# Optimization experiments

Hardware: AMD Instinct MI355X
Metric: run time of the kernel (lower is better)

The kernel has to match this reference:

```python
import jax, jax.numpy as jnp
import numpy as np

N = 100000   # nodes
D = 64       # in_features
E = 1200000  # edges (avg degree ~12)
C = 1.0      # curvature
MIN_NORM = 1e-15
PROJ_EPS = 4e-3  # float32 eps used by HGCN-style PoincareBall.proj


def setup_inputs() -> dict:
    key = jax.random.key(0)
    k1, k2, k3 = jax.random.split(key, 3)
    x = jax.random.normal(k1, (N, D), dtype=jnp.float32) * 0.1
    edge_index = jax.random.randint(k2, (2, E), 0, N, dtype=jnp.int32)
    # GCNConv learned params (lin weight + bias)
    W = jax.random.normal(k3, (D, D), dtype=jnp.float32) / np.sqrt(D)
    b = jnp.zeros((D,), dtype=jnp.float32)
    return {"x": x, "W": W, "b": b, "edge_index": edge_index}


def expmap0(u, c):
    sqrt_c = jnp.sqrt(c)
    u_norm = jnp.maximum(jnp.linalg.norm(u, axis=-1, keepdims=True), MIN_NORM)
    return jnp.tanh(sqrt_c * u_norm) * u / (sqrt_c * u_norm)


def proj(x, c):
    norm = jnp.maximum(jnp.linalg.norm(x, axis=-1, keepdims=True), MIN_NORM)
    maxnorm = (1.0 - PROJ_EPS) / jnp.sqrt(c)
    return jnp.where(norm > maxnorm, x / norm * maxnorm, x)


def gcn_conv(x, W, b, edge_index, n_nodes):
    # PyG GCNConv: h = x @ W; add self-loops; symmetric normalization; scatter-add; + bias
    h = x @ W  # [N, D]
    src, dst = edge_index[0], edge_index[1]
    loops = jnp.arange(n_nodes, dtype=edge_index.dtype)
    s = jnp.concatenate([src, loops])  # [E+N]
    d = jnp.concatenate([dst, loops])
    deg = jax.ops.segment_sum(jnp.ones(s.shape, dtype=h.dtype), d, num_segments=n_nodes)
    deg_inv_sqrt = jnp.where(deg > 0, deg ** -0.5, 0.0)
    norm = deg_inv_sqrt[s] * deg_inv_sqrt[d]  # [E+N]
    msgs = h[s] * norm[:, None]               # gather + scale: [E+N, D]
    out = jax.ops.segment_sum(msgs, d, num_segments=n_nodes)  # scatter-add
    return out + b


def reference(x, W, b, edge_index):
    # Note: original computes logmap0(x) but discards it (conv uses raw x) -- dead code.
    support_t = gcn_conv(x, W, b, edge_index, N)
    return proj(expmap0(support_t, C), C)
```

## Files before the change

kernel.cpp:

```cpp
#include <hip/hip_runtime.h>
#include <hip/hip_bf16.h>

#define DFEAT 64
#define NBSH  8
#define NPB   256
#define EPB   8192

__global__ __launch_bounds__(256) void histA_kernel(const int* __restrict__ ei,
                                                    int* __restrict__ blkhist, int E) {
    __shared__ int h[512];
    int t = threadIdx.x;
    h[t] = 0; h[t + 256] = 0;
    __syncthreads();
    int base = blockIdx.x * EPB;
    #pragma unroll
    for (int i = 0; i < EPB / 256; ++i) {
        int e = base + i * 256 + t;
        if (e < E) atomicAdd(&h[ei[E + e] >> NBSH], 1);
    }
    __syncthreads();
    blkhist[blockIdx.x * 512 + t]       = h[t];
    blkhist[blockIdx.x * 512 + t + 256] = h[t + 256];
}

__global__ __launch_bounds__(512) void scanB_kernel(int* __restrict__ blkhist,
                                                    int* __restrict__ bucketbase, int nblk) {
    __shared__ int lds[512];
    int t = threadIdx.x;
    int run = 0;
    for (int blk = 0; blk < nblk; ++blk) {
        int idx = blk * 512 + t;
        int v = blkhist[idx];
        blkhist[idx] = run;
        run += v;
    }
    lds[t] = run;
    __syncthreads();
    int s = run;
    for (int off = 1; off < 512; off <<= 1) {
        int y = (t >= off) ? lds[t - off] : 0;
        __syncthreads();
        lds[t] += y;
        __syncthreads();
    }
    bucketbase[t] = lds[t] - s;
}

__global__ __launch_bounds__(256) void partC_kernel(const int* __restrict__ ei,
                                                    const int* __restrict__ blkhist,
                                                    const int* __restrict__ bucketbase,
                                                    unsigned* __restrict__ ebuf, int E) {
    __shared__ int cur[512];
    int t = threadIdx.x;
    cur[t]       = bucketbase[t]       + blkhist[blockIdx.x * 512 + t];
    cur[t + 256] = bucketbase[t + 256] + blkhist[blockIdx.x * 512 + t + 256];
    __syncthreads();
    int base = blockIdx.x * EPB;
    #pragma unroll
    for (int i = 0; i < EPB / 256; ++i) {
        int e = base + i * 256 + t;
        if (e < E) {
            int s = ei[e];
            int d = ei[E + e];
            int pos = atomicAdd(&cur[d >> NBSH], 1);
            ebuf[pos] = (unsigned)s | ((unsigned)(d & (NPB - 1)) << 17);
        }
    }
}

__global__ __launch_bounds__(256) void csrD_kernel(const unsigned* __restrict__ ebuf,
                                                   const int* __restrict__ bucketbase,
                                                   int* __restrict__ srcs,
                                                   int* __restrict__ begs,
                                                   int* __restrict__ lens,
                                                   float* __restrict__ dinv, int n) {
    __shared__ int cnt[256];
    __shared__ int tmp[256];
    int t = threadIdx.x;
    int b = blockIdx.x;
    int ebeg = bucketbase[b], eend = bucketbase[b + 1];
    int regionbase = ebeg + b * (4 * NPB);
    cnt[t] = 0;
    __syncthreads();
    for (int e = ebeg + t; e < eend; e += 256)
        atomicAdd(&cnt[ebuf[e] >> 17], 1);
    __syncthreads();
    int nid = (b << NBSH) + t;
    int deg = cnt[t];
    int slots = (nid < n) ? ((deg + 4) & ~3) : 0;
    tmp[t] = slots;
    __syncthreads();
    int s = slots;
    for (int o = 1; o < 256; o <<= 1) {
        int y = (t >= o) ? tmp[t - o] : 0;
        __syncthreads();
        tmp[t] += y;
        __syncthreads();
    }
    int excl = tmp[t] - s;
    if (nid < n) {
        int beg_abs = regionbase + excl;
        begs[nid] = beg_abs;
        lens[nid] = slots;
        dinv[nid] = rsqrtf((float)(deg + 1));
        srcs[beg_abs] = nid;
        for (int k = deg + 1; k < slots; ++k) srcs[beg_abs + k] = n;
    }
    cnt[t] = excl + 1;
    __syncthreads();
    for (int e = ebeg + t; e < eend; e += 256) {
        unsigned v = ebuf[e];
        int pos = atomicAdd(&cnt[v >> 17], 1);
        srcs[regionbase + pos] = (int)(v & 0x1ffffu);
    }
}

__global__ __launch_bounds__(256) void xsprep_kernel(const float* __restrict__ x,
                                                     const float* __restrict__ dinv,
                                                     unsigned* __restrict__ xs, int n) {
    int i = blockIdx.x * blockDim.x + threadIdx.x;
    int total = (n + 1) * 32;
    if (i >= total) return;
    int row = i >> 5, col = i & 31;
    unsigned v = 0;
    if (row < n) {
        float di = dinv[row];
        float f0 = x[row * DFEAT + 2 * col] * di;
        float f1 = x[row * DFEAT + 2 * col + 1] * di;
        unsigned u0 = __float_as_uint(f0); u0 = (u0 + 0x7fffu + ((u0 >> 16) & 1u)) >> 16;
        unsigned u1 = __float_as_uint(f1); u1 = (u1 + 0x7fffu + ((u1 >> 16) & 1u)) >> 16;
        v = (u0 & 0xffffu) | (u1 << 16);
    }
    xs[i] = v;
}

__global__ __launch_bounds__(256) void agg_kernel(const int* __restrict__ begs,
                                                  const int* __restrict__ lens,
                                                  const int* __restrict__ srcs,
                                                  const float* __restrict__ dinv,
                                                  const uint2* __restrict__ xs2,
                                                  const float* __restrict__ W,
                                                  const float* __restrict__ b,
                                                  float* __restrict__ out,
                                                  int n, int nquads) {
    __shared__ float Wl[DFEAT * DFEAT];
    __shared__ float xl[4][DFEAT];
    int t = threadIdx.x;
    #pragma unroll
    for (int i = 0; i < 16; ++i) Wl[i * 256 + t] = W[i * 256 + t];
    __syncthreads();

    int r = t >> 6, lane = t & 63;
    int g = lane >> 4;
    int q = lane & 15;
    float bias = b[lane];

    for (int quad = blockIdx.x; quad < nquads; quad += gridDim.x) {
        int node = quad * 4 + r;
        if (node >= n) continue;

        float f0 = 0, f1 = 0, f2 = 0, f3 = 0;
        int beg = begs[node];
        int end = beg + lens[node];
        for (int base = beg; base < end; base += 64) {
            int m = end - base; if (m > 64) m = 64;
            int idx = 0;
            if (lane < m) idx = srcs[base + lane];
            int quads_ = m >> 2;
            for (int j = 0; j < quads_; ++j) {
                int sv = __shfl(idx, 4 * j + g, 64);
                uint2 d = xs2[(unsigned)sv * 16 + q];
                f0 += __uint_as_float(d.x << 16);
                f1 += __uint_as_float(d.x & 0xffff0000u);
                f2 += __uint_as_float(d.y << 16);
                f3 += __uint_as_float(d.y & 0xffff0000u);
            }
        }
        #pragma unroll
        for (int off = 16; off < 64; off <<= 1) {
            f0 += __shfl_xor(f0, off, 64);
            f1 += __shfl_xor(f1, off, 64);
            f2 += __shfl_xor(f2, off, 64);
            f3 += __shfl_xor(f3, off, 64);
        }
        if (g == 0) {
            float di = dinv[node];
            xl[r][4 * q + 0] = f0 * di;
            xl[r][4 * q + 1] = f1 * di;
            xl[r][4 * q + 2] = f2 * di;
            xl[r][4 * q + 3] = f3 * di;
        }

        float o0 = bias, o1 = 0.0f;
        #pragma unroll
        for (int k = 0; k < DFEAT; k += 2) {
            o0 = fmaf(xl[r][k],     Wl[k * DFEAT + lane],       o0);
            o1 = fmaf(xl[r][k + 1], Wl[(k + 1) * DFEAT + lane], o1);
        }
        float o = o0 + o1;

        float ss = o * o;
        #pragma unroll
        for (int off = 32; off > 0; off >>= 1) ss += __shfl_xor(ss, off, 64);
        float norm = fmaxf(sqrtf(ss), 1e-15f);
        float tn = tanhf(norm);
        float scale = fminf(tn, 1.0f - 4e-3f) / norm;
        out[(long long)node * DFEAT + lane] = o * scale;
    }
}


extern "C" void kernel_launch(void* const* d_in, const int* in_sizes, int n_in,
                              void* d_out, int out_size, void* d_ws, size_t ws_size,
                              hipStream_t stream) {
    const float* x = (const float*)d_in[0];
    const float* W = (const float*)d_in[1];
    const float* b = (const float*)d_in[2];
    const int* ei  = (const int*)d_in[3];

    int n = in_sizes[0] / DFEAT;
    int E = in_sizes[3] / 2;
    int NB = (n + NPB - 1) / NPB;
    int nblk = (E + EPB - 1) / EPB;
    int nquads = (n + 3) / 4;

    int* blkhist    = (int*)d_ws;
    int* bucketbase = blkhist + nblk * 512;
    int* srcs       = bucketbase + 512;
    int* begs       = srcs + E + NB * 4 * NPB;
    int* lens       = begs + n;
    float* dinv     = (float*)(lens + n);
    unsigned* ebuf  = (unsigned*)(dinv + n);
    unsigned* xs    = ebuf;

    float* out = (float*)d_out;

    int aggblocks = 2048;
    if (aggblocks > nquads) aggblocks = nquads;

    histA_kernel <<<nblk, 256, 0, stream>>>(ei, blkhist, E);
    scanB_kernel <<<1, 512, 0, stream>>>(blkhist, bucketbase, nblk);
    partC_kernel <<<nblk, 256, 0, stream>>>(ei, blkhist, bucketbase, ebuf, E);
    csrD_kernel  <<<NB, 256, 0, stream>>>(ebuf, bucketbase, srcs, begs, lens, dinv, n);
    xsprep_kernel<<<((n + 1) * 32 + 255) / 256, 256, 0, stream>>>(x, dinv, xs, n);
    agg_kernel   <<<aggblocks, 256, 0, stream>>>(begs, lens, srcs, dinv,
                                                 (const uint2*)xs, W, b, out, n, nquads);
}
```

Before: 225.6 us.

## Parallelize bucket scan, fuse bf16 prep into CSR build, widen gathers to 16 bytes

The single-block serial scan over all per-block histograms is replaced by a transposed histogram layout, a 512-block per-bucket scan, and a small scan over bucket totals. The xsprep kernel is folded into csrD, which now scales and packs its own rows using dinv held in shared memory. This removes a launch and a reread of dinv. The aggregation kernel loads 8 bf16 features per lane (uint4) for 8 edges per step instead of 4, with a tail path for groups of four. It also gives xs its own aligned workspace region so it no longer aliases ebuf.

After: 228.9 us. About the same (+1.4%).

```diff
diff --git a/kernel.cpp b/kernel.cpp
--- a/kernel.cpp
+++ b/kernel.cpp
@@ -7,7 +7,8 @@
 #define EPB   8192
 
 __global__ __launch_bounds__(256) void histA_kernel(const int* __restrict__ ei,
-                                                    int* __restrict__ blkhist, int E) {
+                                                    int* __restrict__ blkhistT,
+                                                    int E, int nblk) {
     __shared__ int h[512];
     int t = threadIdx.x;
     h[t] = 0; h[t + 256] = 0;
@@ -19,24 +20,37 @@
         if (e < E) atomicAdd(&h[ei[E + e] >> NBSH], 1);
     }
     __syncthreads();
-    blkhist[blockIdx.x * 512 + t]       = h[t];
-    blkhist[blockIdx.x * 512 + t + 256] = h[t + 256];
-}
-
-__global__ __launch_bounds__(512) void scanB_kernel(int* __restrict__ blkhist,
-                                                    int* __restrict__ bucketbase, int nblk) {
+    blkhistT[t * nblk + blockIdx.x]         = h[t];
+    blkhistT[(t + 256) * nblk + blockIdx.x] = h[t + 256];
+}
+
+__global__ __launch_bounds__(256) void scanB1_kernel(int* __restrict__ blkhistT,
+                                                     int* __restrict__ buckettotal, int nblk) {
+    __shared__ int lds[256];
+    int t = threadIdx.x;
+    int b = blockIdx.x;
+    int v = (t < nblk) ? blkhistT[b * nblk + t] : 0;
+    lds[t] = v;
+    __syncthreads();
+    #pragma unroll
+    for (int off = 1; off < 256; off <<= 1) {
+        int y = (t >= off) ? lds[t - off] : 0;
+        __syncthreads();
+        lds[t] += y;
+        __syncthreads();
+    }
+    if (t < nblk) blkhistT[b * nblk + t] = lds[t] - v;
+    if (t == 255) buckettotal[b] = lds[255];
+}
+
+__global__ __launch_bounds__(512) void scanB2_kernel(const int* __restrict__ buckettotal,
+                                                     int* __restrict__ bucketbase) {
     __shared__ int lds[512];
     int t = threadIdx.x;
-    int run = 0;
-    for (int blk = 0; blk < nblk; ++blk) {
-        int idx = blk * 512 + t;
-        int v = blkhist[idx];
-        blkhist[idx] = run;
-        run += v;
-    }
-    lds[t] = run;
-    __syncthreads();
-    int s = run;
+    int s = buckettotal[t];
+    lds[t] = s;
+    __syncthreads();
+    #pragma unroll
     for (int off = 1; off < 512; off <<= 1) {
         int y = (t >= off) ? lds[t - off] : 0;
         __syncthreads();
@@ -44,16 +58,17 @@
         __syncthreads();
     }
     bucketbase[t] = lds[t] - s;
+    if (t == 511) bucketbase[512] = lds[511];
 }
 
 __global__ __launch_bounds__(256) void partC_kernel(const int* __restrict__ ei,
-                                                    const int* __restrict__ blkhist,
+                                                    const int* __restrict__ blkhistT,
                                                     const int* __restrict__ bucketbase,
-                                                    unsigned* __restrict__ ebuf, int E) {
+                                                    unsigned* __restrict__ ebuf, int E, int nblk) {
     __shared__ int cur[512];
     int t = threadIdx.x;
-    cur[t]       = bucketbase[t]       + blkhist[blockIdx.x * 512 + t];
-    cur[t + 256] = bucketbase[t + 256] + blkhist[blockIdx.x * 512 + t + 256];
+    cur[t]       = bucketbase[t]       + blkhistT[t * nblk + blockIdx.x];
+    cur[t + 256] = bucketbase[t + 256] + blkhistT[(t + 256) * nblk + blockIdx.x];
     __syncthreads();
     int base = blockIdx.x * EPB;
     #pragma unroll
@@ -70,12 +85,15 @@
 
 __global__ __launch_bounds__(256) void csrD_kernel(const unsigned* __restrict__ ebuf,
                                                    const int* __restrict__ bucketbase,
+                                                   const float* __restrict__ x,
                                                    int* __restrict__ srcs,
                                                    int* __restrict__ begs,
                                                    int* __restrict__ lens,
-                                                   float* __restrict__ dinv, int n) {
+                                                   float* __restrict__ dinv,
+                                                   unsigned* __restrict__ xs, int n) {
     __shared__ int cnt[256];
     __shared__ int tmp[256];
+    __shared__ float dl[256];
     int t = threadIdx.x;
     int b = blockIdx.x;
     int ebeg = bucketbase[b], eend = bucketbase[b + 1];
@@ -98,11 +116,13 @@
         __syncthreads();
     }
     int excl = tmp[t] - s;
+    float di = rsqrtf((float)(deg + 1));
+    dl[t] = di;
     if (nid < n) {
         int beg_abs = regionbase + excl;
         begs[nid] = beg_abs;
         lens[nid] = slots;
-        dinv[nid] = rsqrtf((float)(deg + 1));
+        dinv[nid] = di;
         srcs[beg_abs] = nid;
         for (int k = deg + 1; k < slots; ++k) srcs[beg_abs + k] = n;
     }
@@ -113,32 +133,29 @@
         int pos = atomicAdd(&cnt[v >> 17], 1);
         srcs[regionbase + pos] = (int)(v & 0x1ffffu);
     }
-}
-
-__global__ __launch_bounds__(256) void xsprep_kernel(const float* __restrict__ x,
-                                                     const float* __restrict__ dinv,
-                                                     unsigned* __restrict__ xs, int n) {
-    int i = blockIdx.x * blockDim.x + threadIdx.x;
-    int total = (n + 1) * 32;
-    if (i >= total) return;
-    int row = i >> 5, col = i & 31;
-    unsigned v = 0;
-    if (row < n) {
-        float di = dinv[row];
-        float f0 = x[row * DFEAT + 2 * col] * di;
-        float f1 = x[row * DFEAT + 2 * col + 1] * di;
-        unsigned u0 = __float_as_uint(f0); u0 = (u0 + 0x7fffu + ((u0 >> 16) & 1u)) >> 16;
-        unsigned u1 = __float_as_uint(f1); u1 = (u1 + 0x7fffu + ((u1 >> 16) & 1u)) >> 16;
-        v = (u0 & 0xffffu) | (u1 << 16);
-    }
-    xs[i] = v;
+    int base_nid = b << NBSH;
+    for (int f = t; f < NPB * 32; f += 256) {
+        int rr = f >> 5, c = f & 31;
+        int node = base_nid + rr;
+        if (node > n) continue;
+        unsigned v = 0;
+        if (node < n) {
+            float dd = dl[rr];
+            float f0 = x[node * DFEAT + 2 * c] * dd;
+            float f1 = x[node * DFEAT + 2 * c + 1] * dd;
+            unsigned u0 = __float_as_uint(f0); u0 = (u0 + 0x7fffu + ((u0 >> 16) & 1u)) >> 16;
+            unsigned u1 = __float_as_uint(f1); u1 = (u1 + 0x7fffu + ((u1 >> 16) & 1u)) >> 16;
+            v = (u0 & 0xffffu) | (u1 << 16);
+        }
+        xs[node * 32 + c] = v;
+    }
 }
 
 __global__ __launch_bounds__(256) void agg_kernel(const int* __restrict__ begs,
                                                   const int* __restrict__ lens,
                                                   const int* __restrict__ srcs,
                                                   const float* __restrict__ dinv,
-                                                  const uint2* __restrict__ xs2,
+                                                  const uint4* __restrict__ xs4,
                                                   const float* __restrict__ W,
                                                   const float* __restrict__ b,
                                                   float* __restrict__ out,
@@ -151,44 +168,70 @@
     __syncthreads();
 
     int r = t >> 6, lane = t & 63;
-    int g = lane >> 4;
-    int q = lane & 15;
+    int g = lane >> 3;
+    int q = lane & 7;
     float bias = b[lane];
 
     for (int quad = blockIdx.x; quad < nquads; quad += gridDim.x) {
         int node = quad * 4 + r;
         if (node >= n) continue;
 
-        float f0 = 0, f1 = 0, f2 = 0, f3 = 0;
+        float f0 = 0, f1 = 0, f2 = 0, f3 = 0, f4 = 0, f5 = 0, f6 = 0, f7 = 0;
         int beg = begs[node];
         int end = beg + lens[node];
         for (int base = beg; base < end; base += 64) {
             int m = end - base; if (m > 64) m = 64;
             int idx = 0;
             if (lane < m) idx = srcs[base + lane];
-            int quads_ = m >> 2;
-            for (int j = 0; j < quads_; ++j) {
-                int sv = __shfl(idx, 4 * j + g, 64);
-                uint2 d = xs2[(unsigned)sv * 16 + q];
+            int octs = m >> 3;
+            for (int j = 0; j < octs; ++j) {
+                int sv = __shfl(idx, 8 * j + g, 64);
+                uint4 d = xs4[(unsigned)sv * 8 + q];
                 f0 += __uint_as_float(d.x << 16);
                 f1 += __uint_as_float(d.x & 0xffff0000u);
                 f2 += __uint_as_float(d.y << 16);
                 f3 += __uint_as_float(d.y & 0xffff0000u);
+                f4 += __uint_as_float(d.z << 16);
+                f5 += __uint_as_float(d.z & 0xffff0000u);
+                f6 += __uint_as_float(d.w << 16);
+                f7 += __uint_as_float(d.w & 0xffff0000u);
             }
+            if (m & 4) {
+                int sv = __shfl(idx, 8 * octs + (g & 3), 64);
+                uint4 d = xs4[(unsigned)sv * 8 + q];
+                if (g < 4) {
+                    f0 += __uint_as_float(d.x << 16);
+                    f1 += __uint_as_float(d.x & 0xffff0000u);
+                    f2 += __uint_as_float(d.y << 16);
+                    f3 += __uint_as_float(d.y & 0xffff0000u);
+                    f4 += __uint_as_float(d.z << 16);
+                    f5 += __uint_as_float(d.z & 0xffff0000u);
+                    f6 += __uint_as_float(d.w << 16);
+                    f7 += __uint_as_float(d.w & 0xffff0000u);
+                }
+            }
         }
         #pragma unroll
-        for (int off = 16; off < 64; off <<= 1) {
+        for (int off = 8; off < 64; off <<= 1) {
             f0 += __shfl_xor(f0, off, 64);
             f1 += __shfl_xor(f1, off, 64);
             f2 += __shfl_xor(f2, off, 64);
             f3 += __shfl_xor(f3, off, 64);
+            f4 += __shfl_xor(f4, off, 64);
+            f5 += __shfl_xor(f5, off, 64);
+            f6 += __shfl_xor(f6, off, 64);
+            f7 += __shfl_xor(f7, off, 64);
         }
         if (g == 0) {
             float di = dinv[node];
-            xl[r][4 * q + 0] = f0 * di;
-            xl[r][4 * q + 1] = f1 * di;
-            xl[r][4 * q + 2] = f2 * di;
-            xl[r][4 * q + 3] = f3 * di;
+            xl[r][8 * q + 0] = f0 * di;
+            xl[r][8 * q + 1] = f1 * di;
+            xl[r][8 * q + 2] = f2 * di;
+            xl[r][8 * q + 3] = f3 * di;
+            xl[r][8 * q + 4] = f4 * di;
+            xl[r][8 * q + 5] = f5 * di;
+            xl[r][8 * q + 6] = f6 * di;
+            xl[r][8 * q + 7] = f7 * di;
         }
 
         float o0 = bias, o1 = 0.0f;
@@ -203,9 +246,8 @@
         #pragma unroll
         for (int off = 32; off > 0; off >>= 1) ss += __shfl_xor(ss, off, 64);
         float norm = fmaxf(sqrtf(ss), 1e-15f);
-        float tn = tanhf(norm);
-        float scale = fminf(tn, 1.0f - 4e-3f) / norm;
-        out[(long long)node * DFEAT + lane] = o * scale;
+        float sc = fminf(tanhf(norm), 1.0f - 4e-3f) / norm;
+        out[(long long)node * DFEAT + lane] = o * sc;
     }
 }
 
@@ -224,25 +266,28 @@
     int nblk = (E + EPB - 1) / EPB;
     int nquads = (n + 3) / 4;
 
-    int* blkhist    = (int*)d_ws;
-    int* bucketbase = blkhist + nblk * 512;
-    int* srcs       = bucketbase + 512;
-    int* begs       = srcs + E + NB * 4 * NPB;
-    int* lens       = begs + n;
-    float* dinv     = (float*)(lens + n);
-    unsigned* ebuf  = (unsigned*)(dinv + n);
-    unsigned* xs    = ebuf;
+    int* blkhistT    = (int*)d_ws;
+    int* buckettotal = blkhistT + 512 * nblk;
+    int* bucketbase  = buckettotal + 512;
+    int* srcs        = bucketbase + 516;
+    int* begs        = srcs + E + NB * 4 * NPB;
+    int* lens        = begs + n;
+    float* dinv      = (float*)(lens + n);
+    size_t xsoff     = (size_t)(((int*)dinv + n) - (int*)d_ws);
+    xsoff            = (xsoff + 31) & ~(size_t)31;
+    unsigned* xs     = (unsigned*)d_ws + xsoff;
+    unsigned* ebuf   = xs + (size_t)(n + 1) * 32;
 
     float* out = (float*)d_out;
 
     int aggblocks = 2048;
     if (aggblocks > nquads) aggblocks = nquads;
 
-    histA_kernel <<<nblk, 256, 0, stream>>>(ei, blkhist, E);
-    scanB_kernel <<<1, 512, 0, stream>>>(blkhist, bucketbase, nblk);
-    partC_kernel <<<nblk, 256, 0, stream>>>(ei, blkhist, bucketbase, ebuf, E);
-    csrD_kernel  <<<NB, 256, 0, stream>>>(ebuf, bucketbase, srcs, begs, lens, dinv, n);
-    xsprep_kernel<<<((n + 1) * 32 + 255) / 256, 256, 0, stream>>>(x, dinv, xs, n);
+    histA_kernel <<<nblk, 256, 0, stream>>>(ei, blkhistT, E, nblk);
+    scanB1_kernel<<<512, 256, 0, stream>>>(blkhistT, buckettotal, nblk);
+    scanB2_kernel<<<1, 512, 0, stream>>>(buckettotal, bucketbase);
+    partC_kernel <<<nblk, 256, 0, stream>>>(ei, blkhistT, bucketbase, ebuf, E, nblk);
+    csrD_kernel  <<<NB, 256, 0, stream>>>(ebuf, bucketbase, x, srcs, begs, lens, dinv, xs, n);
     agg_kernel   <<<aggblocks, 256, 0, stream>>>(begs, lens, srcs, dinv,
-                                                 (const uint2*)xs, W, b, out, n, nquads);
-}
+                                                 (const uint4*)xs, W, b, out, n, nquads);
+}
```
